# Kernel optimization log

Hardware: AMD Instinct MI355X
Metric: run time of the kernel (lower is better)

## Reference

```python
import jax, jax.numpy as jnp
import numpy as np

N, E = 20000, 160000          # nodes, edges
D, ED, H, NH = 32, 16, 64, 4  # node_dim, edge_dim, hidden_dim, num_heads
G, MAXN = 100, 200            # graphs, nodes per graph (equal-size graphs)
HD = H // NH                  # head dim


def setup_inputs() -> dict:
    key = jax.random.key(0)
    ks = jax.random.split(key, 20)
    p = lambda k, shp: jax.random.normal(k, shp, dtype=jnp.float32) * 0.05
    return {
        "x": jax.random.normal(ks[0], (N, D), dtype=jnp.float32),
        "edge_index": jax.random.randint(ks[1], (2, E), 0, N),
        "edge_attr": jax.random.normal(ks[2], (E, ED), dtype=jnp.float32),
        "batch": jnp.arange(N, dtype=jnp.int32) // MAXN,  # 100 graphs x 200 nodes
        "en_w1": p(ks[3], (H, ED)), "en_b1": p(ks[4], (H,)),
        "en_w2": p(ks[5], (D * H, H)), "en_b2": p(ks[6], (D * H,)),
        "root_w": p(ks[7], (D, H)), "conv_b": p(ks[8], (H,)),
        "in_proj_w": p(ks[9], (3 * H, H)), "in_proj_b": p(ks[10], (3 * H,)),
        "out_proj_w": p(ks[11], (H, H)), "out_proj_b": p(ks[12], (H,)),
        "lin1_w": p(ks[13], (H, H)), "lin1_b": p(ks[14], (H,)),
        "lin2_w": p(ks[15], (1, H)), "lin2_b": p(ks[16], (1,)),
    }


def reference(x, edge_index, edge_attr, batch,
              en_w1, en_b1, en_w2, en_b2, root_w, conv_b,
              in_proj_w, in_proj_b, out_proj_w, out_proj_b,
              lin1_w, lin1_b, lin2_w, lin2_b):
    src, dst = edge_index[0], edge_index[1]
    # ---- NNConv: edge MLP -> per-edge weight [E, D, H], gather-matmul-scatter-mean ----
    h = jax.nn.relu(edge_attr @ en_w1.T + en_b1)
    w_e = (h @ en_w2.T + en_b2).reshape(E, D, H)
    msgs = jnp.einsum('ed,edh->eh', x[src], w_e)                 # [E, H]
    agg = jax.ops.segment_sum(msgs, dst, num_segments=N)         # scatter-sum by dest
    cnt = jax.ops.segment_sum(jnp.ones((E,), x.dtype), dst, num_segments=N)
    agg = agg / jnp.maximum(cnt, 1.0)[:, None]                   # mean aggregation
    xh = jax.nn.relu(agg + x @ root_w + conv_b)                  # root weight + bias
    # ---- to_dense_batch (batch is sorted) ----
    counts = jax.ops.segment_sum(jnp.ones((N,), jnp.int32), batch, num_segments=G)
    starts = jnp.concatenate([jnp.zeros((1,), jnp.int32), jnp.cumsum(counts)[:-1]])
    pos = jnp.arange(N, dtype=jnp.int32) - starts[batch]
    dense = jnp.zeros((G, MAXN, H), xh.dtype).at[batch, pos].set(xh)
    mask = jnp.zeros((G, MAXN), bool).at[batch, pos].set(True)
    # ---- MultiheadAttention (self-attn, key_padding_mask = ~mask) ----
    qkv = dense @ in_proj_w.T + in_proj_b                        # [G, MAXN, 3H]
    q, k, v = jnp.split(qkv, 3, axis=-1)
    sh = lambda t: t.reshape(G, MAXN, NH, HD).transpose(0, 2, 1, 3)  # [G, NH, MAXN, HD]
    q, k, v = sh(q), sh(k), sh(v)
    scores = jnp.einsum('gnqd,gnkd->gnqk', q, k) / jnp.sqrt(jnp.float32(HD))
    scores = jnp.where(mask[:, None, None, :], scores, jnp.float32(-1e9))
    attn = jax.nn.softmax(scores, axis=-1)
    ctx = jnp.einsum('gnqk,gnkd->gnqd', attn, v)
    ctx = ctx.transpose(0, 2, 1, 3).reshape(G, MAXN, H)
    attn_out = ctx @ out_proj_w.T + out_proj_b
    # zero out padded positions, masked mean pool
    attn_out = jnp.where(mask[:, :, None], attn_out, 0.0)
    graph_emb = attn_out.sum(axis=1) / mask.sum(axis=1, keepdims=True).astype(attn_out.dtype)
    h1 = jax.nn.relu(graph_emb @ lin1_w.T + lin1_b)
    return (h1 @ lin2_w.T + lin2_b).squeeze(1)                   # [G]
```

## Files before the change

### kernel.cpp

```cpp
#include <hip/hip_runtime.h>
#include <math.h>

#define N_N 20000
#define N_E 160000
#define KA 2112
#define NKB 66

typedef __attribute__((ext_vector_type(8))) short bfrag;
typedef __attribute__((ext_vector_type(4))) float facc;

__device__ __forceinline__ unsigned short f2bf(float f) {
  union { float f; unsigned u; } v; v.f = f;
  unsigned u = v.u;
  return (unsigned short)((u + 0x7FFF + ((u >> 16) & 1)) >> 16);
}
__device__ __forceinline__ unsigned pk2(float a, float b) {
  return (unsigned)f2bf(a) | ((unsigned)f2bf(b) << 16);
}
__device__ __forceinline__ float bflo(unsigned u) {
  union { unsigned u; float f; } v; v.u = u << 16; return v.f;
}
__device__ __forceinline__ float bfhi(unsigned u) {
  union { unsigned u; float f; } v; v.u = u & 0xffff0000u; return v.f;
}

__global__ __launch_bounds__(256) void k_mlp1(const float* __restrict__ ea,
    const float* __restrict__ w1, const float* __restrict__ b1,
    const int* __restrict__ elist, unsigned short* __restrict__ hes) {
  int t = threadIdx.x, w = t >> 6, j = t & 63;
  int p0 = blockIdx.x * 32 + w * 8;
  float wr[16];
#pragma unroll
  for (int i = 0; i < 16; ++i) wr[i] = w1[j * 16 + i];
  float bj = b1[j];
#pragma unroll
  for (int q = 0; q < 8; ++q) {
    int p = p0 + q;
    int e = elist[p];
    const float* a = ea + (size_t)e * 16;
    float s = bj;
#pragma unroll
    for (int i = 0; i < 16; ++i) s += a[i] * wr[i];
    hes[(size_t)p * 64 + j] = f2bf(fmaxf(s, 0.f));
  }
}

__global__ __launch_bounds__(256) void k_hist(const int* __restrict__ eidx,
    int* __restrict__ cnt) {
  int e = blockIdx.x * 256 + threadIdx.x;
  atomicAdd(&cnt[eidx[N_E + e]], 1);
}

__global__ __launch_bounds__(1024) void k_scan(int* __restrict__ hist,
    int* __restrict__ starts) {
  __shared__ int part[1024];
  int t = threadIdx.x;
  const int CH = 20;
  int lo = t * CH;
  int hi = lo + CH; if (hi > N_N) hi = N_N;
  int s = 0;
  for (int i = lo; i < hi; ++i) s += hist[i];
  part[t] = s;
  __syncthreads();
  for (int off = 1; off < 1024; off <<= 1) {
    int v = (t >= off) ? part[t - off] : 0;
    __syncthreads();
    part[t] += v;
    __syncthreads();
  }
  int run = (t == 0) ? 0 : part[t - 1];
  for (int i = lo; i < hi; ++i) {
    int h = hist[i];
    starts[i] = run;
    hist[i] = run;
    run += h;
  }
  if (t == 1023) starts[N_N] = part[1023];
}

__global__ __launch_bounds__(256) void k_scatter(const int* __restrict__ eidx,
    int* __restrict__ cur, int* __restrict__ elist, int* __restrict__ srcl) {
  int e = blockIdx.x * 256 + threadIdx.x;
  int dn = eidx[N_E + e];
  int pos = atomicAdd(&cur[dn], 1);
  elist[pos] = e;
  srcl[pos] = eidx[e];
}

__global__ __launch_bounds__(256) void k_pack(const float* __restrict__ w2,
    const float* __restrict__ b2f, const float* __restrict__ rootw,
    const float* __restrict__ inw,
    unsigned short* __restrict__ Bp, unsigned short* __restrict__ B2p) {
  int idx = blockIdx.x * 256 + threadIdx.x;
  if (idx < 135168) {
    int i = idx & 7, l = (idx >> 3) & 63, cbkb = idx >> 9;
    int cb = cbkb & 3, kb = cbkb >> 2;
    int r = kb * 32 + ((l >> 4) << 3) + i;
    int c = (cb << 4) + (l & 15);
    float v;
    if (r < 2048) { int d = r >> 6, k = r & 63; v = w2[((d << 6) + c) * 64 + k]; }
    else if (r < 2080) v = b2f[((r - 2048) << 6) + c];
    else v = rootw[((r - 2080) << 6) + c];
    Bp[idx] = f2bf(v);
  } else if (idx < 135168 + 12288) {
    int k2 = idx - 135168;
    int i = k2 & 7, l = (k2 >> 3) & 63, cbkb = k2 >> 9;
    int cb = cbkb % 12, kb = cbkb / 12;
    int r = kb * 32 + ((l >> 4) << 3) + i;
    int c = (cb << 4) + (l & 15);
    B2p[k2] = f2bf(inw[c * 64 + r]);
  }
}

#define FMA8(hv, base, xv) \
  acc[base + 0] += xv * bflo(hv.x); acc[base + 1] += xv * bfhi(hv.x); \
  acc[base + 2] += xv * bflo(hv.y); acc[base + 3] += xv * bfhi(hv.y); \
  acc[base + 4] += xv * bflo(hv.z); acc[base + 5] += xv * bfhi(hv.z); \
  acc[base + 6] += xv * bflo(hv.w); acc[base + 7] += xv * bfhi(hv.w);

__global__ __launch_bounds__(256, 4) void k_fused(const float* __restrict__ x,
    const unsigned short* __restrict__ hes, const int* __restrict__ starts,
    const int* __restrict__ srcl,
    const unsigned short* __restrict__ Bp, const unsigned short* __restrict__ B2p,
    const float* __restrict__ convb, const float* __restrict__ inb,
    float* __restrict__ Qb, float* __restrict__ Kb, float* __restrict__ Vb) {
  __shared__ unsigned short Ps[8 * KA];
  __shared__ unsigned short xhT[8 * 68];
  int t = threadIdx.x, w = t >> 6, l = t & 63;
  int n0 = blockIdx.x * 8;
  int d0 = l >> 3, hc = (l & 7) * 8, l31 = l & 31;
#pragma unroll 1
  for (int i4 = 0; i4 < 2; ++i4) {
    int m = w * 2 + i4;
    int n = n0 + m;
    int s0 = starts[n], s1 = starts[n + 1];
    float acc[32];
#pragma unroll
    for (int z = 0; z < 32; ++z) acc[z] = 0.f;
    float xs = 0.f;
#pragma unroll 1
    for (int c0 = s0; c0 < s1; c0 += 64) {
      int srv = 0;
      if (c0 + l < s1) srv = srcl[c0 + l];
      int cc = s1 - c0; if (cc > 64) cc = 64;
#pragma unroll 1
      for (int i = 0; i < cc; i += 4) {
        uint4 h0 = {0,0,0,0}, h1 = {0,0,0,0}, h2 = {0,0,0,0}, h3 = {0,0,0,0};
        float xv0 = 0.f, xv1 = 0.f, xv2 = 0.f, xv3 = 0.f;
        int sr0 = __shfl(srv, i);
        int sr1 = __shfl(srv, i + 1);
        int sr2 = __shfl(srv, i + 2);
        int sr3 = __shfl(srv, i + 3);
        const unsigned short* hp = hes + (size_t)(c0 + i) * 64 + hc;
        h0 = *(const uint4*)hp;
        xv0 = x[(size_t)sr0 * 32 + l31];
        if (i + 1 < cc) { h1 = *(const uint4*)(hp + 64);  xv1 = x[(size_t)sr1 * 32 + l31]; }
        if (i + 2 < cc) { h2 = *(const uint4*)(hp + 128); xv2 = x[(size_t)sr2 * 32 + l31]; }
        if (i + 3 < cc) { h3 = *(const uint4*)(hp + 192); xv3 = x[(size_t)sr3 * 32 + l31]; }
        float a0 = __shfl(xv0, d0),      a1 = __shfl(xv0, d0 + 8);
        float a2 = __shfl(xv0, d0 + 16), a3 = __shfl(xv0, d0 + 24);
        FMA8(h0, 0, a0) FMA8(h0, 8, a1) FMA8(h0, 16, a2) FMA8(h0, 24, a3)
        float b0 = __shfl(xv1, d0),      b1 = __shfl(xv1, d0 + 8);
        float b2 = __shfl(xv1, d0 + 16), b3 = __shfl(xv1, d0 + 24);
        FMA8(h1, 0, b0) FMA8(h1, 8, b1) FMA8(h1, 16, b2) FMA8(h1, 24, b3)
        float c0f = __shfl(xv2, d0),      c1f = __shfl(xv2, d0 + 8);
        float c2f = __shfl(xv2, d0 + 16), c3f = __shfl(xv2, d0 + 24);
        FMA8(h2, 0, c0f) FMA8(h2, 8, c1f) FMA8(h2, 16, c2f) FMA8(h2, 24, c3f)
        float e0 = __shfl(xv3, d0),      e1 = __shfl(xv3, d0 + 8);
        float e2 = __shfl(xv3, d0 + 16), e3 = __shfl(xv3, d0 + 24);
        FMA8(h3, 0, e0) FMA8(h3, 8, e1) FMA8(h3, 16, e2) FMA8(h3, 24, e3)
        xs += xv0 + xv1 + xv2 + xv3;
      }
    }
    int s = m;
#pragma unroll
    for (int q = 0; q < 4; ++q) {
      int sc = (l + 64 * q) ^ s;
      uint4 o;
      o.x = pk2(acc[q * 8 + 0], acc[q * 8 + 1]);
      o.y = pk2(acc[q * 8 + 2], acc[q * 8 + 3]);
      o.z = pk2(acc[q * 8 + 4], acc[q * 8 + 5]);
      o.w = pk2(acc[q * 8 + 6], acc[q * 8 + 7]);
      *(uint4*)(Ps + m * KA + sc * 8) = o;
    }
    if (l < 32) {
      int cnt = s1 - s0; if (cnt < 1) cnt = 1;
      int c1 = (256 + (l >> 3)) ^ s, c2 = (260 + (l >> 3)) ^ s;
      Ps[m * KA + c1 * 8 + (l & 7)] = f2bf(xs);
      Ps[m * KA + c2 * 8 + (l & 7)] = f2bf(x[(size_t)n * 32 + l] * (float)cnt);
    }
  }
  __syncthreads();
  int col = l & 15, sub = l >> 4;
  int arow = col & 7;
  const bfrag* Bb = (const bfrag*)Bp + w * 64 + l;
  facc ac = {0.f, 0.f, 0.f, 0.f};
#pragma unroll 4
  for (int kb = 0; kb < NKB; ++kb) {
    int sc = ((kb << 2) + sub) ^ arow;
    bfrag af = *(const bfrag*)(Ps + arow * KA + sc * 8);
    ac = __builtin_amdgcn_mfma_f32_16x16x32_bf16(af, Bb[kb * 256], ac, 0, 0, 0);
  }
  float cv = convb[w * 16 + col];
#pragma unroll
  for (int j = 0; j < 4; ++j) {
    int m = sub * 4 + j;
    if (m < 8) {
      int n = n0 + m;
      int cnt = starts[n + 1] - starts[n]; if (cnt < 1) cnt = 1;
      float inv = 1.f / (float)cnt;
      xhT[m * 68 + w * 16 + col] = f2bf(fmaxf(ac[j] * inv + cv, 0.f));
    }
  }
  __syncthreads();
  bfrag af0 = *(const bfrag*)&xhT[(col & 7) * 68 + sub * 8];
  bfrag af1 = *(const bfrag*)&xhT[(col & 7) * 68 + 32 + sub * 8];
  const bfrag* B2b = (const bfrag*)B2p + l;
#pragma unroll
  for (int c3 = 0; c3 < 3; ++c3) {
    int cb = w * 3 + c3;
    facc qa = {0.f, 0.f, 0.f, 0.f};
    qa = __builtin_amdgcn_mfma_f32_16x16x32_bf16(af0, B2b[cb * 64], qa, 0, 0, 0);
    qa = __builtin_amdgcn_mfma_f32_16x16x32_bf16(af1, B2b[(12 + cb) * 64], qa, 0, 0, 0);
#pragma unroll
    for (int j = 0; j < 4; ++j) {
      int m = sub * 4 + j;
      if (m < 8) {
        int n = n0 + m;
        int g = n / 200, p = n - g * 200;
        int c = cb * 16 + col;
        float v = qa[j] + inb[c];
        int part = c >> 6, rem = c & 63, hh = rem >> 4, dd = rem & 15;
        float* dst = (part == 0) ? Qb : (part == 1 ? Kb : Vb);
        dst[(((size_t)g * 4 + hh) * 200 + p) * 16 + dd] = v;
      }
    }
  }
}

__global__ __launch_bounds__(256) void k_attn(const float* __restrict__ Qb,
    const float* __restrict__ Kb, const float* __restrict__ Vb,
    float* __restrict__ ctx) {
  __shared__ unsigned short Ks[224 * 24];
  __shared__ unsigned short Vt[16 * 232];
  __shared__ unsigned short Pl[4][16 * 40];
  int t = threadIdx.x;
  int gh = blockIdx.x >> 1, half = blockIdx.x & 1;
  size_t base = (size_t)gh * 3200;
  for (int idx = t; idx < 224 * 16; idx += 256) {
    int row = idx >> 4, d = idx & 15;
    float kv = (row < 200) ? Kb[base + idx] : 0.f;
    float vv = (row < 200) ? Vb[base + idx] : 0.f;
    Ks[row * 24 + d] = f2bf(kv);
    Vt[d * 232 + row] = f2bf(vv);
  }
  __syncthreads();
  int w = t >> 6, l = t & 63;
  int sub = l >> 4, col = l & 15;
  int qlo = half * 7, qhi = half ? 13 : 7;
  for (int qt = qlo + w; qt < qhi; qt += 4) {
    bfrag qf = {0, 0, 0, 0, 0, 0, 0, 0};
    int q = qt * 16 + col;
    if (sub < 2 && q < 200) {
      const float* qp = Qb + base + q * 16 + sub * 8;
      float4 qa = *(const float4*)qp;
      float4 qb = *(const float4*)(qp + 4);
      qf[0] = (short)f2bf(qa.x); qf[1] = (short)f2bf(qa.y);
      qf[2] = (short)f2bf(qa.z); qf[3] = (short)f2bf(qa.w);
      qf[4] = (short)f2bf(qb.x); qf[5] = (short)f2bf(qb.y);
      qf[6] = (short)f2bf(qb.z); qf[7] = (short)f2bf(qb.w);
    }
    facc o = {0.f, 0.f, 0.f, 0.f};
    float srow0 = 0.f, srow1 = 0.f, srow2 = 0.f, srow3 = 0.f;
    for (int kt2 = 0; kt2 < 7; ++kt2) {
      int kt0 = kt2 * 2, kt1 = kt0 + 1;
      bfrag kf0 = {0, 0, 0, 0, 0, 0, 0, 0};
      bfrag kf1 = {0, 0, 0, 0, 0, 0, 0, 0};
      if (sub < 2) {
        kf0 = *(const bfrag*)&Ks[(kt0 * 16 + col) * 24 + sub * 8];
        kf1 = *(const bfrag*)&Ks[(kt1 * 16 + col) * 24 + sub * 8];
      }
      facc z = {0.f, 0.f, 0.f, 0.f};
      facc s0 = __builtin_amdgcn_mfma_f32_16x16x32_bf16(qf, kf0, z, 0, 0, 0);
      facc s1 = __builtin_amdgcn_mfma_f32_16x16x32_bf16(qf, kf1, z, 0, 0, 0);
      bool ok0 = (kt0 * 16 + col) < 200;
      bool ok1 = (kt1 * 16 + col) < 200;
#pragma unroll
      for (int j = 0; j < 4; ++j) {
        float e0 = ok0 ? __expf(s0[j] * 0.25f) : 0.f;
        float e1 = ok1 ? __expf(s1[j] * 0.25f) : 0.f;
        if (j == 0) { srow0 += e0 + e1; } else if (j == 1) { srow1 += e0 + e1; }
        else if (j == 2) { srow2 += e0 + e1; } else { srow3 += e0 + e1; }
        int qr = (sub << 2) + j;
        Pl[w][qr * 40 + col] = f2bf(e0);
        Pl[w][qr * 40 + 16 + col] = f2bf(e1);
      }
      bfrag pf = *(const bfrag*)&Pl[w][col * 40 + sub * 8];
      bfrag vf = *(const bfrag*)&Vt[col * 232 + kt2 * 32 + sub * 8];
      o = __builtin_amdgcn_mfma_f32_16x16x32_bf16(pf, vf, o, 0, 0, 0);
    }
#pragma unroll
    for (int off = 1; off < 16; off <<= 1) {
      srow0 += __shfl_xor(srow0, off);
      srow1 += __shfl_xor(srow1, off);
      srow2 += __shfl_xor(srow2, off);
      srow3 += __shfl_xor(srow3, off);
    }
#pragma unroll
    for (int j = 0; j < 4; ++j) {
      int qq = qt * 16 + (sub << 2) + j;
      float sr = (j == 0) ? srow0 : (j == 1) ? srow1 : (j == 2) ? srow2 : srow3;
      if (qq < 200) ctx[base + qq * 16 + col] = o[j] / sr;
    }
  }
}

__global__ __launch_bounds__(256) void k_head(const float* __restrict__ ctx,
    const float* __restrict__ ow, const float* __restrict__ ob,
    const float* __restrict__ w1, const float* __restrict__ b1,
    const float* __restrict__ w2, const float* __restrict__ b2,
    float* __restrict__ out) {
  __shared__ float pool[4][64];
  __shared__ float ms[64], es[64];
  int g = blockIdx.x, t = threadIdx.x;
  int q = t >> 6, c = t & 63;
  int hh = c >> 4, dd = c & 15;
  const float* cb = ctx + (((size_t)g * 4 + hh) * 200) * 16 + dd;
  float s = 0.f;
  for (int p = q; p < 200; p += 4) s += cb[p * 16];
  pool[q][c] = s;
  __syncthreads();
  if (t < 64) {
    float sm = pool[0][t] + pool[1][t] + pool[2][t] + pool[3][t];
    ms[t] = sm * (1.f / 200.f);
  }
  __syncthreads();
  if (t < 64) {
    float e = ob[t];
    for (int j = 0; j < 64; ++j) e += ow[t * 64 + j] * ms[j];
    es[t] = e;
  }
  __syncthreads();
  if (t < 64) {
    float h1 = b1[t];
    for (int j = 0; j < 64; ++j) h1 += w1[t * 64 + j] * es[j];
    h1 = fmaxf(h1, 0.f);
    float pr = h1 * w2[t];
    for (int off = 32; off >= 1; off >>= 1) pr += __shfl_xor(pr, off);
    if (t == 0) out[g] = pr + b2[0];
  }
}

extern "C" void kernel_launch(void* const* d_in, const int* in_sizes, int n_in,
                              void* d_out, int out_size, void* d_ws, size_t ws_size,
                              hipStream_t stream) {
  (void)in_sizes; (void)n_in;
  const float* x      = (const float*)d_in[0];
  const int*   eidx   = (const int*)d_in[1];
  const float* ea     = (const float*)d_in[2];
  const float* en_w1  = (const float*)d_in[4];
  const float* en_b1  = (const float*)d_in[5];
  const float* en_w2  = (const float*)d_in[6];
  const float* en_b2  = (const float*)d_in[7];
  const float* root_w = (const float*)d_in[8];
  const float* conv_b = (const float*)d_in[9];
  const float* in_w   = (const float*)d_in[10];
  const float* in_b   = (const float*)d_in[11];
  const float* out_w  = (const float*)d_in[12];
  const float* out_b  = (const float*)d_in[13];
  const float* l1w    = (const float*)d_in[14];
  const float* l1b    = (const float*)d_in[15];
  const float* l2w    = (const float*)d_in[16];
  const float* l2b    = (const float*)d_in[17];
  float* out = (float*)d_out;

  char* w = (char*)d_ws;
  unsigned short* hes = (unsigned short*)w;
  float* Qb  = (float*)(w + 20480000);
  float* Kb  = (float*)(w + 25600000);
  float* Vb  = (float*)(w + 30720000);
  float* ctx = (float*)(w + 35840000);
  char* r3 = w + 40960000;
  unsigned short* Bp  = (unsigned short*)r3;
  unsigned short* B2p = (unsigned short*)(r3 + 270336);
  int* starts = (int*)(r3 + 270336 + 24576);
  int* elist  = starts + (N_N + 4);
  int* srcl   = elist + N_E;
  int* cursor = srcl + N_E;
  size_t need = 40960000 + 270336 + 24576
              + (size_t)(N_N + 4) * 4 + 2 * (size_t)N_E * 4 + (size_t)N_N * 4;
  if (ws_size < need || out_size < 100) return;

  hipMemsetAsync(cursor, 0, N_N * 4, stream);
  k_pack<<<580, 256, 0, stream>>>(en_w2, en_b2, root_w, in_w, Bp, B2p);
  k_hist<<<N_E / 256, 256, 0, stream>>>(eidx, cursor);
  k_scan<<<1, 1024, 0, stream>>>(cursor, starts);
  k_scatter<<<N_E / 256, 256, 0, stream>>>(eidx, cursor, elist, srcl);
  k_mlp1<<<5000, 256, 0, stream>>>(ea, en_w1, en_b1, elist, hes);
  k_fused<<<2500, 256, 0, stream>>>(x, hes, starts, srcl, Bp, B2p,
                                    conv_b, in_b, Qb, Kb, Vb);
  k_attn<<<800, 256, 0, stream>>>(Qb, Kb, Vb, ctx);
  k_head<<<100, 256, 0, stream>>>(ctx, out_w, out_b, l1w, l1b, l2w, l2b, out);
}
```

Baseline: 180.7 us.

## Merge preprocessing kernels into one cooperative kernel with grid syncs

Replaces the memset, pack, histogram, scan, scatter and edge-MLP launches with a single cooperative kernel of 512 blocks that separates the phases with grid.sync. The single-block scan becomes a two-level parallel chunk scan. The aim is to remove the per-launch overhead and serialization of several small kernels and the slow single-block scan. In exchange it adds grid-wide barrier cost, limits the edge-MLP stage to a fixed 512-block grid, and relies on cooperative launch residency.

```diff
diff --git a/kernel.cpp b/kernel.cpp
--- a/kernel.cpp
+++ b/kernel.cpp
@@ -1,5 +1,8 @@
 #include <hip/hip_runtime.h>
+#include <hip/hip_cooperative_groups.h>
 #include <math.h>
+
+namespace cg = cooperative_groups;
 
 #define N_N 20000
 #define N_E 160000
@@ -24,91 +27,117 @@
   union { unsigned u; float f; } v; v.u = u & 0xffff0000u; return v.f;
 }
 
-__global__ __launch_bounds__(256) void k_mlp1(const float* __restrict__ ea,
-    const float* __restrict__ w1, const float* __restrict__ b1,
-    const int* __restrict__ elist, unsigned short* __restrict__ hes) {
-  int t = threadIdx.x, w = t >> 6, j = t & 63;
-  int p0 = blockIdx.x * 32 + w * 8;
-  float wr[16];
-#pragma unroll
-  for (int i = 0; i < 16; ++i) wr[i] = w1[j * 16 + i];
-  float bj = b1[j];
-#pragma unroll
-  for (int q = 0; q < 8; ++q) {
-    int p = p0 + q;
-    int e = elist[p];
-    const float* a = ea + (size_t)e * 16;
-    float s = bj;
-#pragma unroll
-    for (int i = 0; i < 16; ++i) s += a[i] * wr[i];
-    hes[(size_t)p * 64 + j] = f2bf(fmaxf(s, 0.f));
-  }
-}
-
-__global__ __launch_bounds__(256) void k_hist(const int* __restrict__ eidx,
-    int* __restrict__ cnt) {
-  int e = blockIdx.x * 256 + threadIdx.x;
-  atomicAdd(&cnt[eidx[N_E + e]], 1);
-}
-
-__global__ __launch_bounds__(1024) void k_scan(int* __restrict__ hist,
-    int* __restrict__ starts) {
-  __shared__ int part[1024];
-  int t = threadIdx.x;
-  const int CH = 20;
-  int lo = t * CH;
-  int hi = lo + CH; if (hi > N_N) hi = N_N;
-  int s = 0;
-  for (int i = lo; i < hi; ++i) s += hist[i];
-  part[t] = s;
-  __syncthreads();
-  for (int off = 1; off < 1024; off <<= 1) {
-    int v = (t >= off) ? part[t - off] : 0;
+__global__ __launch_bounds__(256, 2) void k_pre(
+    const float* __restrict__ ea, const float* __restrict__ w1,
+    const float* __restrict__ b1, const int* __restrict__ eidx,
+    const float* __restrict__ w2, const float* __restrict__ b2f,
+    const float* __restrict__ rootw, const float* __restrict__ inw,
+    unsigned short* __restrict__ Bp, unsigned short* __restrict__ B2p,
+    int* __restrict__ cursor, int* __restrict__ starts,
+    int* __restrict__ elist, int* __restrict__ srcl,
+    unsigned short* __restrict__ hes, int* __restrict__ chunkAux) {
+  cg::grid_group grid = cg::this_grid();
+  __shared__ int sc[256];
+  int t = threadIdx.x, b = blockIdx.x;
+  int gtid = b * 256 + t;
+  const int GT = 512 * 256;
+  const int nchunks = (N_N + 255) / 256;
+
+  for (int idx = gtid; idx < 135168 + 12288; idx += GT) {
+    if (idx < 135168) {
+      int i = idx & 7, l = (idx >> 3) & 63, cbkb = idx >> 9;
+      int cb = cbkb & 3, kb = cbkb >> 2;
+      int r = kb * 32 + ((l >> 4) << 3) + i;
+      int c = (cb << 4) + (l & 15);
+      float v;
+      if (r < 2048) { int d = r >> 6, k = r & 63; v = w2[((d << 6) + c) * 64 + k]; }
+      else if (r < 2080) v = b2f[((r - 2048) << 6) + c];
+      else v = rootw[((r - 2080) << 6) + c];
+      Bp[idx] = f2bf(v);
+    } else {
+      int k2 = idx - 135168;
+      int i = k2 & 7, l = (k2 >> 3) & 63, cbkb = k2 >> 9;
+      int cb = cbkb % 12, kb = cbkb / 12;
+      int r = kb * 32 + ((l >> 4) << 3) + i;
+      int c = (cb << 4) + (l & 15);
+      B2p[k2] = f2bf(inw[c * 64 + r]);
+    }
+  }
+  for (int i = gtid; i < N_N; i += GT) cursor[i] = 0;
+  grid.sync();
+
+  for (int e = gtid; e < N_E; e += GT) atomicAdd(&cursor[eidx[N_E + e]], 1);
+  grid.sync();
+
+  if (b < nchunks) {
+    int i = b * 256 + t;
+    int v = (i < N_N) ? cursor[i] : 0;
+    sc[t] = v;
     __syncthreads();
-    part[t] += v;
+    for (int off = 1; off < 256; off <<= 1) {
+      int u = (t >= off) ? sc[t - off] : 0;
+      __syncthreads();
+      sc[t] += u;
+      __syncthreads();
+    }
+    if (i < N_N) starts[i] = sc[t] - v;
+    if (t == 255) chunkAux[b] = sc[255];
+  }
+  grid.sync();
+
+  if (b == 0) {
+    int v = (t < nchunks) ? chunkAux[t] : 0;
+    sc[t] = v;
     __syncthreads();
-  }
-  int run = (t == 0) ? 0 : part[t - 1];
-  for (int i = lo; i < hi; ++i) {
-    int h = hist[i];
-    starts[i] = run;
-    hist[i] = run;
-    run += h;
-  }
-  if (t == 1023) starts[N_N] = part[1023];
-}
-
-__global__ __launch_bounds__(256) void k_scatter(const int* __restrict__ eidx,
-    int* __restrict__ cur, int* __restrict__ elist, int* __restrict__ srcl) {
-  int e = blockIdx.x * 256 + threadIdx.x;
-  int dn = eidx[N_E + e];
-  int pos = atomicAdd(&cur[dn], 1);
-  elist[pos] = e;
-  srcl[pos] = eidx[e];
-}
-
-__global__ __launch_bounds__(256) void k_pack(const float* __restrict__ w2,
-    const float* __restrict__ b2f, const float* __restrict__ rootw,
-    const float* __restrict__ inw,
-    unsigned short* __restrict__ Bp, unsigned short* __restrict__ B2p) {
-  int idx = blockIdx.x * 256 + threadIdx.x;
-  if (idx < 135168) {
-    int i = idx & 7, l = (idx >> 3) & 63, cbkb = idx >> 9;
-    int cb = cbkb & 3, kb = cbkb >> 2;
-    int r = kb * 32 + ((l >> 4) << 3) + i;
-    int c = (cb << 4) + (l & 15);
-    float v;
-    if (r < 2048) { int d = r >> 6, k = r & 63; v = w2[((d << 6) + c) * 64 + k]; }
-    else if (r < 2080) v = b2f[((r - 2048) << 6) + c];
-    else v = rootw[((r - 2080) << 6) + c];
-    Bp[idx] = f2bf(v);
-  } else if (idx < 135168 + 12288) {
-    int k2 = idx - 135168;
-    int i = k2 & 7, l = (k2 >> 3) & 63, cbkb = k2 >> 9;
-    int cb = cbkb % 12, kb = cbkb / 12;
-    int r = kb * 32 + ((l >> 4) << 3) + i;
-    int c = (cb << 4) + (l & 15);
-    B2p[k2] = f2bf(inw[c * 64 + r]);
+    for (int off = 1; off < 256; off <<= 1) {
+      int u = (t >= off) ? sc[t - off] : 0;
+      __syncthreads();
+      sc[t] += u;
+      __syncthreads();
+    }
+    if (t < nchunks) chunkAux[t] = sc[t] - v;
+  }
+  grid.sync();
+
+  if (b < nchunks) {
+    int i = b * 256 + t;
+    if (i < N_N) {
+      int s = starts[i] + chunkAux[b];
+      starts[i] = s;
+      cursor[i] = s;
+    }
+  }
+  if (gtid == 0) starts[N_N] = N_E;
+  grid.sync();
+
+  for (int e = gtid; e < N_E; e += GT) {
+    int dn = eidx[N_E + e];
+    int pos = atomicAdd(&cursor[dn], 1);
+    elist[pos] = e;
+    srcl[pos] = eidx[e];
+  }
+  grid.sync();
+
+  {
+    int w = t >> 6, j = t & 63;
+    float wr[16];
+#pragma unroll
+    for (int i = 0; i < 16; ++i) wr[i] = w1[j * 16 + i];
+    float bj = b1[j];
+    int wid = b * 4 + w;
+#pragma unroll 1
+    for (int p0 = wid * 8; p0 < N_E; p0 += 2048 * 8) {
+#pragma unroll
+      for (int q = 0; q < 8; ++q) {
+        int p = p0 + q;
+        int e = elist[p];
+        const float* a = ea + (size_t)e * 16;
+        float s = bj;
+#pragma unroll
+        for (int i = 0; i < 16; ++i) s += a[i] * wr[i];
+        hes[(size_t)p * 64 + j] = f2bf(fmaxf(s, 0.f));
+      }
+    }
   }
 }
 
@@ -175,13 +204,13 @@
     int s = m;
 #pragma unroll
     for (int q = 0; q < 4; ++q) {
-      int sc = (l + 64 * q) ^ s;
+      int scr = (l + 64 * q) ^ s;
       uint4 o;
       o.x = pk2(acc[q * 8 + 0], acc[q * 8 + 1]);
       o.y = pk2(acc[q * 8 + 2], acc[q * 8 + 3]);
       o.z = pk2(acc[q * 8 + 4], acc[q * 8 + 5]);
       o.w = pk2(acc[q * 8 + 6], acc[q * 8 + 7]);
-      *(uint4*)(Ps + m * KA + sc * 8) = o;
+      *(uint4*)(Ps + m * KA + scr * 8) = o;
     }
     if (l < 32) {
       int cnt = s1 - s0; if (cnt < 1) cnt = 1;
@@ -197,8 +226,8 @@
   facc ac = {0.f, 0.f, 0.f, 0.f};
 #pragma unroll 4
   for (int kb = 0; kb < NKB; ++kb) {
-    int sc = ((kb << 2) + sub) ^ arow;
-    bfrag af = *(const bfrag*)(Ps + arow * KA + sc * 8);
+    int scr = ((kb << 2) + sub) ^ arow;
+    bfrag af = *(const bfrag*)(Ps + arow * KA + scr * 8);
     ac = __builtin_amdgcn_mfma_f32_16x16x32_bf16(af, Bb[kb * 256], ac, 0, 0, 0);
   }
   float cv = convb[w * 16 + col];
@@ -387,16 +416,16 @@
   int* elist  = starts + (N_N + 4);
   int* srcl   = elist + N_E;
   int* cursor = srcl + N_E;
+  int* chunkAux = cursor + N_N;
   size_t need = 40960000 + 270336 + 24576
-              + (size_t)(N_N + 4) * 4 + 2 * (size_t)N_E * 4 + (size_t)N_N * 4;
+              + (size_t)(N_N + 4) * 4 + 2 * (size_t)N_E * 4 + (size_t)N_N * 4 + 1024;
   if (ws_size < need || out_size < 100) return;
 
-  hipMemsetAsync(cursor, 0, N_N * 4, stream);
-  k_pack<<<580, 256, 0, stream>>>(en_w2, en_b2, root_w, in_w, Bp, B2p);
-  k_hist<<<N_E / 256, 256, 0, stream>>>(eidx, cursor);
-  k_scan<<<1, 1024, 0, stream>>>(cursor, starts);
-  k_scatter<<<N_E / 256, 256, 0, stream>>>(eidx, cursor, elist, srcl);
-  k_mlp1<<<5000, 256, 0, stream>>>(ea, en_w1, en_b1, elist, hes);
+  void* args[] = { (void*)&ea, (void*)&en_w1, (void*)&en_b1, (void*)&eidx,
+                   (void*)&en_w2, (void*)&en_b2, (void*)&root_w, (void*)&in_w,
+                   (void*)&Bp, (void*)&B2p, (void*)&cursor, (void*)&starts,
+                   (void*)&elist, (void*)&srcl, (void*)&hes, (void*)&chunkAux };
+  hipLaunchCooperativeKernel((const void*)k_pre, dim3(512), dim3(256), args, 0, stream);
   k_fused<<<2500, 256, 0, stream>>>(x, hes, starts, srcl, Bp, B2p,
                                     conv_b, in_b, Qb, Kb, Vb);
   k_attn<<<800, 256, 0, stream>>>(Qb, Kb, Vb, ctx);
```

New measurement: 480.0 us. 166% more time.
